# Performance work log

Hardware: AMD Instinct MI355X
Metric: run time of the kernel (lower is better)

## Reference

```python
import jax, jax.numpy as jnp
import numpy as np

B, T, H = 4, 4096, 2048
NUM_HEADS, HEAD_DIM = 16, 128


def setup_inputs() -> dict:
    key = jax.random.key(0)
    k1, k2, k3 = jax.random.split(key, 3)
    hidden = jax.random.normal(k1, (B, T, H), dtype=jnp.float32)
    # Linear(H -> 3H): store weight as [H, 3H] for x @ W
    w_qkv = jax.random.normal(k2, (H, 3 * H), dtype=jnp.float32) * (1.0 / np.sqrt(H))
    b_qkv = jax.random.normal(k3, (3 * H,), dtype=jnp.float32) * 0.02
    return {"hidden": hidden, "w_qkv": w_qkv, "b_qkv": b_qkv}


def _to_heads(x):
    # (B, T, H) -> (B, num_heads, T, head_dim)
    b, t, _ = x.shape
    return x.reshape(b, t, NUM_HEADS, HEAD_DIM).transpose(0, 2, 1, 3)


def reference(hidden, w_qkv, b_qkv):
    # fused QKV projection: (B,T,H) @ (H,3H) + (3H,)
    qkv = jnp.einsum('bth,hd->btd', hidden, w_qkv) + b_qkv
    q, k, v = jnp.split(qkv, 3, axis=-1)
    return _to_heads(q), _to_heads(k), _to_heads(v)
```

## Files before the change

kernel.cpp:

```cpp
#include <hip/hip_runtime.h>
#include <hip/hip_bf16.h>
#include <stdint.h>

#define M_DIM 16384
#define K_DIM 2048
#define N_DIM 6144
#define NT    32

typedef __attribute__((ext_vector_type(8))) short bf16x8;
typedef __attribute__((ext_vector_type(8))) unsigned short u16x8;
typedef __attribute__((ext_vector_type(4))) float f32x4;

__device__ __forceinline__ unsigned short f2bf(float f) {
  unsigned int u = __float_as_uint(f);
  u += 0x7FFFu + ((u >> 16) & 1u);
  return (unsigned short)(u >> 16);
}

__device__ __forceinline__ void load_lds16(const void* g, void* l) {
  __builtin_amdgcn_global_load_lds((const __attribute__((address_space(1))) void*)g,
                                   (__attribute__((address_space(3))) void*)l, 16, 0, 0);
}

#define FENCE asm volatile("" ::: "memory")
#define BAR   do { FENCE; __builtin_amdgcn_s_barrier(); FENCE; } while (0)
#define LGKM0 do { asm volatile("s_waitcnt lgkmcnt(0)" ::: "memory"); \
                   __builtin_amdgcn_sched_barrier(0); } while (0)

__global__ __launch_bounds__(256) void cvt_hidden(const float* __restrict__ in,
                                                  unsigned short* __restrict__ out) {
  unsigned int base = blockIdx.x * 256u + threadIdx.x;
  #pragma unroll
  for (int i = 0; i < 16; ++i) {
    unsigned int fi = i * 524288u + base;
    float4 v = reinterpret_cast<const float4*>(in)[fi];
    ushort4 o;
    o.x = f2bf(v.x); o.y = f2bf(v.y); o.z = f2bf(v.z); o.w = f2bf(v.w);
    reinterpret_cast<ushort4*>(out)[fi] = o;
  }
}

__global__ __launch_bounds__(256) void cvt_w(const float* __restrict__ w,
                                             unsigned short* __restrict__ wt) {
  __shared__ float tile[64][69];
  const int k0 = blockIdx.x * 64;
  const int n0 = blockIdx.y * 64;
  const int t = threadIdx.x;
  #pragma unroll
  for (int i = 0; i < 4; ++i) {
    int idx = i * 256 + t;
    int row = idx >> 4, c4 = idx & 15;
    float4 v = *reinterpret_cast<const float4*>(&w[(size_t)(k0 + row) * N_DIM + n0 + c4 * 4]);
    tile[row][c4 * 4 + 0] = v.x; tile[row][c4 * 4 + 1] = v.y;
    tile[row][c4 * 4 + 2] = v.z; tile[row][c4 * 4 + 3] = v.w;
  }
  __syncthreads();
  #pragma unroll
  for (int i = 0; i < 2; ++i) {
    int idx = i * 256 + t;
    int n = idx >> 3, k8 = idx & 7;
    u16x8 v;
    #pragma unroll
    for (int e = 0; e < 8; ++e) v[e] = f2bf(tile[k8 * 8 + e][n]);
    *reinterpret_cast<u16x8*>(&wt[(size_t)(n0 + n) * K_DIM + k0 + k8 * 8]) = v;
  }
}

__global__ __launch_bounds__(512, 2) void gemm_qkv_8ph(const unsigned short* __restrict__ A,
                                                       const unsigned short* __restrict__ Bt,
                                                       const float* __restrict__ bias,
                                                       float* __restrict__ out) {
  extern __shared__ __align__(16) char smem[];
  const int tid = threadIdx.x, lane = tid & 63, wid = tid >> 6;
  const int wm = wid >> 2, wn = wid & 3;

  const int bid = blockIdx.x;
  const int swz = (bid & 7) * 192 + (bid >> 3);
  const int bm = swz / 24, bn = swz % 24;
  const int m0 = bm * 256, n0 = bn * 256;

  const int srow  = tid >> 3;
  const int sslot = (tid & 7) ^ ((tid >> 3) & 7);
  const unsigned short* gA = A  + (size_t)(m0 + srow) * K_DIM + sslot * 8;
  const unsigned short* gB = Bt + (size_t)(n0 + srow) * K_DIM + sslot * 8;

  const int r15 = lane & 15, q4 = lane >> 4, x7 = lane & 7;
  const int abase = (wm * 128 + r15) * 128;
  const int bbase = (wn * 64  + r15) * 128;
  const int sw0 = ((0 + q4) ^ x7) * 16;
  const int sw1 = ((4 + q4) ^ x7) * 16;

  f32x4 acc[2][2][4][2] = {};
  bf16x8 a[4][2], b0[2][2], b1[2][2];

  #define STAGE_T(gsrc, ldsbase)                                              \
    { const unsigned short* _g = (gsrc); char* _l = (ldsbase);                \
      load_lds16(_g,                       _l +     wid * 1024);              \
      load_lds16(_g + (size_t)64  * K_DIM, _l + 8192  + wid * 1024);          \
      load_lds16(_g + (size_t)128 * K_DIM, _l + 16384 + wid * 1024);          \
      load_lds16(_g + (size_t)192 * K_DIM, _l + 24576 + wid * 1024); }

  {
    char* A0 = smem;          char* B0 = smem + 32768;
    char* A1 = smem + 65536;  char* B1 = smem + 98304;
    STAGE_T(gB +  0, B0); STAGE_T(gA +  0, A0);
    STAGE_T(gB + 64, B1); STAGE_T(gA + 64, A1);
    asm volatile("s_waitcnt vmcnt(8)" ::: "memory");
    BAR;
  }

  for (int t = 0; t < NT; ++t) {
    char* Ab = smem + (t & 1) * 65536;
    char* Bb = Ab + 32768;
    const bool st = (t + 2 < NT);

    #pragma unroll
    for (int mi = 0; mi < 4; ++mi) {
      const char* p = Ab + abase + mi * (16 * 128);
      a[mi][0] = *(const bf16x8*)(p + sw0);
      a[mi][1] = *(const bf16x8*)(p + sw1);
    }
    #pragma unroll
    for (int ni = 0; ni < 2; ++ni) {
      const char* p = Bb + bbase + ni * (16 * 128);
      b0[ni][0] = *(const bf16x8*)(p + sw0);
      b0[ni][1] = *(const bf16x8*)(p + sw1);
    }
    BAR; LGKM0;
    __builtin_amdgcn_s_setprio(1);
    #pragma unroll
    for (int mi = 0; mi < 4; ++mi)
      #pragma unroll
      for (int ni = 0; ni < 2; ++ni) {
        acc[0][0][mi][ni] = __builtin_amdgcn_mfma_f32_16x16x32_bf16(a[mi][0], b0[ni][0], acc[0][0][mi][ni], 0, 0, 0);
        acc[0][0][mi][ni] = __builtin_amdgcn_mfma_f32_16x16x32_bf16(a[mi][1], b0[ni][1], acc[0][0][mi][ni], 0, 0, 0);
      }
    __builtin_amdgcn_s_setprio(0);
    BAR;

    #pragma unroll
    for (int ni = 0; ni < 2; ++ni) {
      const char* p = Bb + bbase + (32 + ni * 16) * 128;
      b1[ni][0] = *(const bf16x8*)(p + sw0);
      b1[ni][1] = *(const bf16x8*)(p + sw1);
    }
    BAR; LGKM0;
    __builtin_amdgcn_s_setprio(1);
    #pragma unroll
    for (int mi = 0; mi < 4; ++mi)
      #pragma unroll
      for (int ni = 0; ni < 2; ++ni) {
        acc[0][1][mi][ni] = __builtin_amdgcn_mfma_f32_16x16x32_bf16(a[mi][0], b1[ni][0], acc[0][1][mi][ni], 0, 0, 0);
        acc[0][1][mi][ni] = __builtin_amdgcn_mfma_f32_16x16x32_bf16(a[mi][1], b1[ni][1], acc[0][1][mi][ni], 0, 0, 0);
      }
    __builtin_amdgcn_s_setprio(0);
    BAR;

    #pragma unroll
    for (int mi = 0; mi < 4; ++mi) {
      const char* p = Ab + abase + (64 + mi * 16) * 128;
      a[mi][0] = *(const bf16x8*)(p + sw0);
      a[mi][1] = *(const bf16x8*)(p + sw1);
    }
    if (st) STAGE_T(gB + (size_t)(t + 2) * 64, Bb);
    BAR; LGKM0;
    __builtin_amdgcn_s_setprio(1);
    #pragma unroll
    for (int mi = 0; mi < 4; ++mi)
      #pragma unroll
      for (int ni = 0; ni < 2; ++ni) {
        acc[1][0][mi][ni] = __builtin_amdgcn_mfma_f32_16x16x32_bf16(a[mi][0], b0[ni][0], acc[1][0][mi][ni], 0, 0, 0);
        acc[1][0][mi][ni] = __builtin_amdgcn_mfma_f32_16x16x32_bf16(a[mi][1], b0[ni][1], acc[1][0][mi][ni], 0, 0, 0);
      }
    __builtin_amdgcn_s_setprio(0);
    BAR;

    if (st) STAGE_T(gA + (size_t)(t + 2) * 64, Ab);
    BAR; LGKM0;
    __builtin_amdgcn_s_setprio(1);
    #pragma unroll
    for (int mi = 0; mi < 4; ++mi)
      #pragma unroll
      for (int ni = 0; ni < 2; ++ni) {
        acc[1][1][mi][ni] = __builtin_amdgcn_mfma_f32_16x16x32_bf16(a[mi][0], b1[ni][0], acc[1][1][mi][ni], 0, 0, 0);
        acc[1][1][mi][ni] = __builtin_amdgcn_mfma_f32_16x16x32_bf16(a[mi][1], b1[ni][1], acc[1][1][mi][ni], 0, 0, 0);
      }
    __builtin_amdgcn_s_setprio(0);
    if (st) { asm volatile("s_waitcnt vmcnt(8)" ::: "memory"); }
    else    { asm volatile("s_waitcnt vmcnt(0)" ::: "memory"); }
    BAR;
  }
  #undef STAGE_T

  #pragma unroll
  for (int qn = 0; qn < 2; ++qn)
    #pragma unroll
    for (int ni = 0; ni < 2; ++ni) {
      const int col = n0 + wn * 64 + qn * 32 + ni * 16 + r15;
      const float bv = bias[col];
      const int which = col >> 11, head = (col & 2047) >> 7, hd = col & 127;
      float* ob = out + (size_t)which * 33554432 + (size_t)head * 524288 + hd;
      #pragma unroll
      for (int qm = 0; qm < 2; ++qm)
        #pragma unroll
        for (int mi = 0; mi < 4; ++mi)
          #pragma unroll
          for (int r = 0; r < 4; ++r) {
            const int mrow = m0 + wm * 128 + qm * 64 + mi * 16 + q4 * 4 + r;
            const int bb_ = mrow >> 12, tt = mrow & 4095;
            ob[(size_t)bb_ * 8388608 + (size_t)tt * 128] = acc[qm][qn][mi][ni][r] + bv;
          }
    }
}

__global__ __launch_bounds__(256) void naive_qkv(const float* __restrict__ h,
                                                 const float* __restrict__ w,
                                                 const float* __restrict__ bias,
                                                 float* __restrict__ out) {
  const int m = blockIdx.x;
  const int n = blockIdx.y * 256 + threadIdx.x;
  const float* hr = h + (size_t)m * K_DIM;
  float acc = bias[n];
  for (int k = 0; k < K_DIM; ++k) acc = fmaf(hr[k], w[(size_t)k * N_DIM + n], acc);
  const int which = n >> 11, head = (n & 2047) >> 7, hd = n & 127;
  const int bb = m >> 12, tt = m & 4095;
  out[(size_t)which * 33554432 + (size_t)bb * 8388608 + (size_t)head * 524288 +
      (size_t)tt * 128 + hd] = acc;
}

extern "C" void kernel_launch(void* const* d_in, const int* in_sizes, int n_in,
                              void* d_out, int out_size, void* d_ws, size_t ws_size,
                              hipStream_t stream) {
  const float* hidden = (const float*)d_in[0];
  const float* w_qkv  = (const float*)d_in[1];
  const float* b_qkv  = (const float*)d_in[2];
  float* out = (float*)d_out;

  const size_t needA = (size_t)M_DIM * K_DIM * 2;
  const size_t needB = (size_t)N_DIM * K_DIM * 2;
  if (ws_size >= needA + needB) {
    unsigned short* Abf = (unsigned short*)d_ws;
    unsigned short* Wt  = (unsigned short*)((char*)d_ws + needA);
    (void)hipFuncSetAttribute((const void*)gemm_qkv_8ph,
                              hipFuncAttributeMaxDynamicSharedMemorySize, 131072);
    cvt_hidden<<<2048, 256, 0, stream>>>(hidden, Abf);
    cvt_w<<<dim3(32, 96), 256, 0, stream>>>(w_qkv, Wt);
    gemm_qkv_8ph<<<1536, 512, 131072, stream>>>(Abf, Wt, b_qkv, out);
  } else {
    naive_qkv<<<dim3(16384, 24), 256, 0, stream>>>(hidden, w_qkv, b_qkv, out);
  }
}
```

Measured before the change: 498.2 us.

## Make GEMM persistent over six tiles, prefetch next tile during epilogue, vectorize stores

The GEMM now launches 256 workgroups, one per CU, and each loops over six 256x256 output tiles, with a new XCD-aware tile mapping. Loads for the next tile's first K-steps are issued before the current tile's epilogue so the stores overlap with prefetch. The MFMA operand order is swapped so each lane holds four consecutive columns, which allows float4 bias loads and float4 output stores instead of scalar ones. The cost is a fixed 256-block grid that assumes 256 CUs and one block per CU, giving up the previous two-blocks-per-CU occupancy, plus a hand-tuned vmcnt wait that must match the number of outstanding loads.

```diff
diff --git a/kernel.cpp b/kernel.cpp
--- a/kernel.cpp
+++ b/kernel.cpp
@@ -6,6 +6,7 @@
 #define K_DIM 2048
 #define N_DIM 6144
 #define NT    32
+#define NTILES 6
 
 typedef __attribute__((ext_vector_type(8))) short bf16x8;
 typedef __attribute__((ext_vector_type(8))) unsigned short u16x8;
@@ -74,24 +75,16 @@
   const int tid = threadIdx.x, lane = tid & 63, wid = tid >> 6;
   const int wm = wid >> 2, wn = wid & 3;
 
-  const int bid = blockIdx.x;
-  const int swz = (bid & 7) * 192 + (bid >> 3);
-  const int bm = swz / 24, bn = swz % 24;
-  const int m0 = bm * 256, n0 = bn * 256;
+  const int xcd = blockIdx.x & 7;
+  const int lcl = blockIdx.x >> 3;
 
   const int srow  = tid >> 3;
   const int sslot = (tid & 7) ^ ((tid >> 3) & 7);
-  const unsigned short* gA = A  + (size_t)(m0 + srow) * K_DIM + sslot * 8;
-  const unsigned short* gB = Bt + (size_t)(n0 + srow) * K_DIM + sslot * 8;
-
   const int r15 = lane & 15, q4 = lane >> 4, x7 = lane & 7;
   const int abase = (wm * 128 + r15) * 128;
   const int bbase = (wn * 64  + r15) * 128;
   const int sw0 = ((0 + q4) ^ x7) * 16;
   const int sw1 = ((4 + q4) ^ x7) * 16;
-
-  f32x4 acc[2][2][4][2] = {};
-  bf16x8 a[4][2], b0[2][2], b1[2][2];
 
   #define STAGE_T(gsrc, ldsbase)                                              \
     { const unsigned short* _g = (gsrc); char* _l = (ldsbase);                \
@@ -100,117 +93,155 @@
       load_lds16(_g + (size_t)128 * K_DIM, _l + 16384 + wid * 1024);          \
       load_lds16(_g + (size_t)192 * K_DIM, _l + 24576 + wid * 1024); }
 
-  {
-    char* A0 = smem;          char* B0 = smem + 32768;
-    char* A1 = smem + 65536;  char* B1 = smem + 98304;
-    STAGE_T(gB +  0, B0); STAGE_T(gA +  0, A0);
-    STAGE_T(gB + 64, B1); STAGE_T(gA + 64, A1);
-    asm volatile("s_waitcnt vmcnt(8)" ::: "memory");
-    BAR;
-  }
-
-  for (int t = 0; t < NT; ++t) {
-    char* Ab = smem + (t & 1) * 65536;
-    char* Bb = Ab + 32768;
-    const bool st = (t + 2 < NT);
-
+  #define TILE_PARAMS(j, m0_, n0_, gA_, gB_)                                  \
+    { const int idx = (j) * 32 + lcl;                                         \
+      const int bm = xcd * 8 + idx / 24, bn = idx % 24;                       \
+      m0_ = bm * 256; n0_ = bn * 256;                                         \
+      gA_ = A  + (size_t)(m0_ + srow) * K_DIM + sslot * 8;                    \
+      gB_ = Bt + (size_t)(n0_ + srow) * K_DIM + sslot * 8; }
+
+  char* A0 = smem;          char* B0 = smem + 32768;
+  char* A1 = smem + 65536;  char* B1 = smem + 98304;
+
+  int m0, n0;
+  const unsigned short *gA, *gB;
+  TILE_PARAMS(0, m0, n0, gA, gB);
+  STAGE_T(gB +  0, B0); STAGE_T(gA +  0, A0);
+  STAGE_T(gB + 64, B1); STAGE_T(gA + 64, A1);
+  asm volatile("s_waitcnt vmcnt(8)" ::: "memory");
+  BAR;
+
+  for (int j = 0; j < NTILES; ++j) {
+    float4 bv4[2][2];
     #pragma unroll
-    for (int mi = 0; mi < 4; ++mi) {
-      const char* p = Ab + abase + mi * (16 * 128);
-      a[mi][0] = *(const bf16x8*)(p + sw0);
-      a[mi][1] = *(const bf16x8*)(p + sw1);
+    for (int qn = 0; qn < 2; ++qn)
+      #pragma unroll
+      for (int ni = 0; ni < 2; ++ni)
+        bv4[qn][ni] = *reinterpret_cast<const float4*>(
+            &bias[n0 + wn * 64 + qn * 32 + ni * 16 + q4 * 4]);
+
+    f32x4 acc[2][2][4][2] = {};
+    bf16x8 a[4][2], b0[2][2], b1[2][2];
+
+    for (int t = 0; t < NT; ++t) {
+      char* Ab = smem + (t & 1) * 65536;
+      char* Bb = Ab + 32768;
+      const bool st = (t + 2 < NT);
+
+      #pragma unroll
+      for (int mi = 0; mi < 4; ++mi) {
+        const char* p = Ab + abase + mi * (16 * 128);
+        a[mi][0] = *(const bf16x8*)(p + sw0);
+        a[mi][1] = *(const bf16x8*)(p + sw1);
+      }
+      #pragma unroll
+      for (int ni = 0; ni < 2; ++ni) {
+        const char* p = Bb + bbase + ni * (16 * 128);
+        b0[ni][0] = *(const bf16x8*)(p + sw0);
+        b0[ni][1] = *(const bf16x8*)(p + sw1);
+      }
+      BAR; LGKM0;
+      __builtin_amdgcn_s_setprio(1);
+      #pragma unroll
+      for (int mi = 0; mi < 4; ++mi)
+        #pragma unroll
+        for (int ni = 0; ni < 2; ++ni) {
+          acc[0][0][mi][ni] = __builtin_amdgcn_mfma_f32_16x16x32_bf16(b0[ni][0], a[mi][0], acc[0][0][mi][ni], 0, 0, 0);
+          acc[0][0][mi][ni] = __builtin_amdgcn_mfma_f32_16x16x32_bf16(b0[ni][1], a[mi][1], acc[0][0][mi][ni], 0, 0, 0);
+        }
+      __builtin_amdgcn_s_setprio(0);
+      BAR;
+
+      #pragma unroll
+      for (int ni = 0; ni < 2; ++ni) {
+        const char* p = Bb + bbase + (32 + ni * 16) * 128;
+        b1[ni][0] = *(const bf16x8*)(p + sw0);
+        b1[ni][1] = *(const bf16x8*)(p + sw1);
+      }
+      BAR; LGKM0;
+      __builtin_amdgcn_s_setprio(1);
+      #pragma unroll
+      for (int mi = 0; mi < 4; ++mi)
+        #pragma unroll
+        for (int ni = 0; ni < 2; ++ni) {
+          acc[0][1][mi][ni] = __builtin_amdgcn_mfma_f32_16x16x32_bf16(b1[ni][0], a[mi][0], acc[0][1][mi][ni], 0, 0, 0);
+          acc[0][1][mi][ni] = __builtin_amdgcn_mfma_f32_16x16x32_bf16(b1[ni][1], a[mi][1], acc[0][1][mi][ni], 0, 0, 0);
+        }
+      __builtin_amdgcn_s_setprio(0);
+      BAR;
+
+      #pragma unroll
+      for (int mi = 0; mi < 4; ++mi) {
+        const char* p = Ab + abase + (64 + mi * 16) * 128;
+        a[mi][0] = *(const bf16x8*)(p + sw0);
+        a[mi][1] = *(const bf16x8*)(p + sw1);
+      }
+      if (st) STAGE_T(gB + (size_t)(t + 2) * 64, Bb);
+      BAR; LGKM0;
+      __builtin_amdgcn_s_setprio(1);
+      #pragma unroll
+      for (int mi = 0; mi < 4; ++mi)
+        #pragma unroll
+        for (int ni = 0; ni < 2; ++ni) {
+          acc[1][0][mi][ni] = __builtin_amdgcn_mfma_f32_16x16x32_bf16(b0[ni][0], a[mi][0], acc[1][0][mi][ni], 0, 0, 0);
+          acc[1][0][mi][ni] = __builtin_amdgcn_mfma_f32_16x16x32_bf16(b0[ni][1], a[mi][1], acc[1][0][mi][ni], 0, 0, 0);
+        }
+      __builtin_amdgcn_s_setprio(0);
+      BAR;
+
+      if (st) STAGE_T(gA + (size_t)(t + 2) * 64, Ab);
+      BAR; LGKM0;
+      __builtin_amdgcn_s_setprio(1);
+      #pragma unroll
+      for (int mi = 0; mi < 4; ++mi)
+        #pragma unroll
+        for (int ni = 0; ni < 2; ++ni) {
+          acc[1][1][mi][ni] = __builtin_amdgcn_mfma_f32_16x16x32_bf16(b1[ni][0], a[mi][0], acc[1][1][mi][ni], 0, 0, 0);
+          acc[1][1][mi][ni] = __builtin_amdgcn_mfma_f32_16x16x32_bf16(b1[ni][1], a[mi][1], acc[1][1][mi][ni], 0, 0, 0);
+        }
+      __builtin_amdgcn_s_setprio(0);
+      if (st) { asm volatile("s_waitcnt vmcnt(8)" ::: "memory"); }
+      else    { asm volatile("s_waitcnt vmcnt(0)" ::: "memory"); }
+      BAR;
     }
+
+    const int cm0 = m0, cn0 = n0;
+    if (j + 1 < NTILES) {
+      TILE_PARAMS(j + 1, m0, n0, gA, gB);
+      STAGE_T(gB +  0, B0); STAGE_T(gA +  0, A0);
+      STAGE_T(gB + 64, B1); STAGE_T(gA + 64, A1);
+    }
+
     #pragma unroll
-    for (int ni = 0; ni < 2; ++ni) {
-      const char* p = Bb + bbase + ni * (16 * 128);
-      b0[ni][0] = *(const bf16x8*)(p + sw0);
-      b0[ni][1] = *(const bf16x8*)(p + sw1);
+    for (int qm = 0; qm < 2; ++qm)
+      #pragma unroll
+      for (int mi = 0; mi < 4; ++mi) {
+        const int m = cm0 + wm * 128 + qm * 64 + mi * 16 + r15;
+        const int bb_ = m >> 12, tt = m & 4095;
+        float* orow = out + (size_t)bb_ * 8388608 + (size_t)tt * 128;
+        #pragma unroll
+        for (int qn = 0; qn < 2; ++qn)
+          #pragma unroll
+          for (int ni = 0; ni < 2; ++ni) {
+            const int col = cn0 + wn * 64 + qn * 32 + ni * 16 + q4 * 4;
+            const int which = col >> 11, head = (col & 2047) >> 7, hd = col & 127;
+            float4 v;
+            v.x = acc[qm][qn][mi][ni][0] + bv4[qn][ni].x;
+            v.y = acc[qm][qn][mi][ni][1] + bv4[qn][ni].y;
+            v.z = acc[qm][qn][mi][ni][2] + bv4[qn][ni].z;
+            v.w = acc[qm][qn][mi][ni][3] + bv4[qn][ni].w;
+            *reinterpret_cast<float4*>(orow + (size_t)which * 33554432 +
+                                       (size_t)head * 524288 + hd) = v;
+          }
+      }
+
+    if (j + 1 < NTILES) {
+      asm volatile("s_waitcnt vmcnt(40)" ::: "memory");
+      BAR;
     }
-    BAR; LGKM0;
-    __builtin_amdgcn_s_setprio(1);
-    #pragma unroll
-    for (int mi = 0; mi < 4; ++mi)
-      #pragma unroll
-      for (int ni = 0; ni < 2; ++ni) {
-        acc[0][0][mi][ni] = __builtin_amdgcn_mfma_f32_16x16x32_bf16(a[mi][0], b0[ni][0], acc[0][0][mi][ni], 0, 0, 0);
-        acc[0][0][mi][ni] = __builtin_amdgcn_mfma_f32_16x16x32_bf16(a[mi][1], b0[ni][1], acc[0][0][mi][ni], 0, 0, 0);
-      }
-    __builtin_amdgcn_s_setprio(0);
-    BAR;
-
-    #pragma unroll
-    for (int ni = 0; ni < 2; ++ni) {
-      const char* p = Bb + bbase + (32 + ni * 16) * 128;
-      b1[ni][0] = *(const bf16x8*)(p + sw0);
-      b1[ni][1] = *(const bf16x8*)(p + sw1);
-    }
-    BAR; LGKM0;
-    __builtin_amdgcn_s_setprio(1);
-    #pragma unroll
-    for (int mi = 0; mi < 4; ++mi)
-      #pragma unroll
-      for (int ni = 0; ni < 2; ++ni) {
-        acc[0][1][mi][ni] = __builtin_amdgcn_mfma_f32_16x16x32_bf16(a[mi][0], b1[ni][0], acc[0][1][mi][ni], 0, 0, 0);
-        acc[0][1][mi][ni] = __builtin_amdgcn_mfma_f32_16x16x32_bf16(a[mi][1], b1[ni][1], acc[0][1][mi][ni], 0, 0, 0);
-      }
-    __builtin_amdgcn_s_setprio(0);
-    BAR;
-
-    #pragma unroll
-    for (int mi = 0; mi < 4; ++mi) {
-      const char* p = Ab + abase + (64 + mi * 16) * 128;
-      a[mi][0] = *(const bf16x8*)(p + sw0);
-      a[mi][1] = *(const bf16x8*)(p + sw1);
-    }
-    if (st) STAGE_T(gB + (size_t)(t + 2) * 64, Bb);
-    BAR; LGKM0;
-    __builtin_amdgcn_s_setprio(1);
-    #pragma unroll
-    for (int mi = 0; mi < 4; ++mi)
-      #pragma unroll
-      for (int ni = 0; ni < 2; ++ni) {
-        acc[1][0][mi][ni] = __builtin_amdgcn_mfma_f32_16x16x32_bf16(a[mi][0], b0[ni][0], acc[1][0][mi][ni], 0, 0, 0);
-        acc[1][0][mi][ni] = __builtin_amdgcn_mfma_f32_16x16x32_bf16(a[mi][1], b0[ni][1], acc[1][0][mi][ni], 0, 0, 0);
-      }
-    __builtin_amdgcn_s_setprio(0);
-    BAR;
-
-    if (st) STAGE_T(gA + (size_t)(t + 2) * 64, Ab);
-    BAR; LGKM0;
-    __builtin_amdgcn_s_setprio(1);
-    #pragma unroll
-    for (int mi = 0; mi < 4; ++mi)
-      #pragma unroll
-      for (int ni = 0; ni < 2; ++ni) {
-        acc[1][1][mi][ni] = __builtin_amdgcn_mfma_f32_16x16x32_bf16(a[mi][0], b1[ni][0], acc[1][1][mi][ni], 0, 0, 0);
-        acc[1][1][mi][ni] = __builtin_amdgcn_mfma_f32_16x16x32_bf16(a[mi][1], b1[ni][1], acc[1][1][mi][ni], 0, 0, 0);
-      }
-    __builtin_amdgcn_s_setprio(0);
-    if (st) { asm volatile("s_waitcnt vmcnt(8)" ::: "memory"); }
-    else    { asm volatile("s_waitcnt vmcnt(0)" ::: "memory"); }
-    BAR;
   }
   #undef STAGE_T
-
-  #pragma unroll
-  for (int qn = 0; qn < 2; ++qn)
-    #pragma unroll
-    for (int ni = 0; ni < 2; ++ni) {
-      const int col = n0 + wn * 64 + qn * 32 + ni * 16 + r15;
-      const float bv = bias[col];
-      const int which = col >> 11, head = (col & 2047) >> 7, hd = col & 127;
-      float* ob = out + (size_t)which * 33554432 + (size_t)head * 524288 + hd;
-      #pragma unroll
-      for (int qm = 0; qm < 2; ++qm)
-        #pragma unroll
-        for (int mi = 0; mi < 4; ++mi)
-          #pragma unroll
-          for (int r = 0; r < 4; ++r) {
-            const int mrow = m0 + wm * 128 + qm * 64 + mi * 16 + q4 * 4 + r;
-            const int bb_ = mrow >> 12, tt = mrow & 4095;
-            ob[(size_t)bb_ * 8388608 + (size_t)tt * 128] = acc[qm][qn][mi][ni][r] + bv;
-          }
-    }
+  #undef TILE_PARAMS
 }
 
 __global__ __launch_bounds__(256) void naive_qkv(const float* __restrict__ h,
@@ -245,7 +276,7 @@
                               hipFuncAttributeMaxDynamicSharedMemorySize, 131072);
     cvt_hidden<<<2048, 256, 0, stream>>>(hidden, Abf);
     cvt_w<<<dim3(32, 96), 256, 0, stream>>>(w_qkv, Wt);
-    gemm_qkv_8ph<<<1536, 512, 131072, stream>>>(Abf, Wt, b_qkv, out);
+    gemm_qkv_8ph<<<256, 512, 131072, stream>>>(Abf, Wt, b_qkv, out);
   } else {
     naive_qkv<<<dim3(16384, 24), 256, 0, stream>>>(hidden, w_qkv, b_qkv, out);
   }
```

Result: faster. 479.7 us (-3.7%).
